# Kernel optimization log

Measured on AMD Instinct MI355X. Metric: run time of the kernel, lower is better.

The kernel has to match this reference:

```python
import jax, jax.numpy as jnp
import numpy as np

MARGIN = 0.2
EPS = 1e-12  # F.normalize eps


def _l2norm(x, axis):
    n = jnp.linalg.norm(x, axis=axis, keepdims=True)
    return x / jnp.maximum(n, EPS)


def setup_inputs() -> dict:
    key = jax.random.key(0)
    k1, k2, k3, k4 = jax.random.split(key, 4)
    B, L_im, L_s, D = 256, 37, 33, 1024
    im_set = jax.random.normal(k1, (B, L_im, D), dtype=jnp.float32)
    s_seq = jax.random.normal(k2, (B, L_s, D), dtype=jnp.float32)
    # realistic valid lengths (>= a few regions/words, <= max)
    im_len = jax.random.randint(k3, (B,), 10, L_im + 1, dtype=jnp.int32)
    s_len = jax.random.randint(k4, (B,), 8, L_s + 1, dtype=jnp.int32)
    return {"im_set": im_set, "s_seq": s_seq, "im_len": im_len, "s_len": s_len}


def _aggr_similarity(im_set, s_seq, im_len, s_len):
    # l2-normalize feature dim, then drop CLS region / special tokens
    im = _l2norm(im_set, axis=2)[:, 1:, :]          # [B, Li, D]
    s = _l2norm(s_seq, axis=2)[:, 1:-2, :]          # [B, Ls, D]
    im_l = im_len - 1
    s_l = s_len - 3
    Li, Ls = im.shape[1], s.shape[1]
    # cross-batch alignment scores: [B_im, B_s, Li, Ls]
    align = jnp.einsum('bid,cjd->bcij', im, s)
    im_invalid = jnp.arange(Li)[None, :] >= im_l[:, None]   # [B, Li]
    s_invalid = jnp.arange(Ls)[None, :] >= s_l[:, None]     # [B, Ls]
    mask = im_invalid[:, None, :, None] | s_invalid[None, :, None, :]
    align = jnp.where(mask, 0.0, align)
    # 'MrSw': max over image regions, sum over sentence words
    return align.max(axis=2).sum(axis=2)             # [B_im, B_s]


def _contrastive_loss(scores):
    B = scores.shape[0]
    diag = jnp.diagonal(scores)                      # [B]
    cost_s = jnp.maximum(MARGIN + scores - diag[:, None], 0.0)
    cost_im = jnp.maximum(MARGIN + scores - diag[None, :], 0.0)
    eye = jnp.eye(B, dtype=bool)
    cost_s = jnp.where(eye, 0.0, cost_s)
    cost_im = jnp.where(eye, 0.0, cost_im)
    # max_violation=True: hardest negatives
    return cost_s.max(axis=1).sum() + cost_im.max(axis=0).sum()


def reference(im_set, s_seq, im_len, s_len):
    scores = _aggr_similarity(im_set, s_seq, im_len, s_len)
    return _contrastive_loss(scores)
```

## Files before the change

### kernel.cpp

```cpp
#include <hip/hip_runtime.h>
#include <hip/hip_bf16.h>


typedef __attribute__((ext_vector_type(8))) short bf16x8;
typedef __attribute__((ext_vector_type(4))) float f32x4;

#define NB   256
#define DIM  1024
#define LI   36
#define LIP  36
#define LS   30
#define LSP  32

static __device__ inline ushort f2bf(float x) {
    union { __hip_bfloat16 h; ushort u; } cvt;
    cvt.h = __float2bfloat16(x);
    return cvt.u;
}

static __device__ __forceinline__ void gload_lds16(const void* g, void* l) {
    __builtin_amdgcn_global_load_lds(
        (const __attribute__((address_space(1))) void*)g,
        (__attribute__((address_space(3))) void*)l, 16, 0, 0);
}

__global__ __launch_bounds__(256) void normalize_pack(
    const float* __restrict__ im, const float* __restrict__ sq,
    short* __restrict__ imp, short* __restrict__ sp)
{
    const int gw   = (blockIdx.x * 256 + threadIdx.x) >> 6;
    const int lane = threadIdx.x & 63;
    const int NIM  = NB * LI;

    const float* src[2];
    short* dst[2];
    #pragma unroll
    for (int rr = 0; rr < 2; ++rr) {
        const int row = gw * 2 + rr;
        if (row < NIM) {
            int b = row / LI, i = row - b * LI;
            dst[rr] = imp + (size_t)row * DIM;
            src[rr] = im + ((size_t)b * 37 + i + 1) * DIM;
        } else {
            int g2 = row - NIM;
            int b = g2 >> 5, j = g2 & 31;
            dst[rr] = sp + (size_t)g2 * DIM;
            src[rr] = (j < LS) ? (sq + ((size_t)b * 33 + j + 1) * DIM)
                               : nullptr;
        }
    }

    float4 v[2][4];
    float ss[2] = {0.f, 0.f};
    #pragma unroll
    for (int rr = 0; rr < 2; ++rr) {
        if (src[rr]) {
            const float4* s4 = (const float4*)src[rr];
            #pragma unroll
            for (int t = 0; t < 4; ++t) {
                float4 x = s4[lane + 64 * t];
                v[rr][t] = x;
                ss[rr] += x.x * x.x + x.y * x.y + x.z * x.z + x.w * x.w;
            }
        }
    }
    #pragma unroll
    for (int o = 32; o >= 1; o >>= 1) {
        ss[0] += __shfl_xor(ss[0], o, 64);
        ss[1] += __shfl_xor(ss[1], o, 64);
    }
    #pragma unroll
    for (int rr = 0; rr < 2; ++rr) {
        if (src[rr]) {
            const float scale = 1.0f / fmaxf(sqrtf(ss[rr]), 1e-12f);
            ushort4* d4 = (ushort4*)dst[rr];
            #pragma unroll
            for (int t = 0; t < 4; ++t) {
                float4 x = v[rr][t];
                ushort4 o;
                o.x = f2bf(x.x * scale);
                o.y = f2bf(x.y * scale);
                o.z = f2bf(x.z * scale);
                o.w = f2bf(x.w * scale);
                d4[lane + 64 * t] = o;
            }
        } else {
            uint4 z = {0u, 0u, 0u, 0u};
            uint4* d4 = (uint4*)dst[rr];
            d4[lane] = z;
            d4[lane + 64] = z;
        }
    }
}

__global__ __launch_bounds__(256, 2) void gemm_scores(
    const short* __restrict__ imp, const short* __restrict__ sp,
    const int* __restrict__ im_len, const int* __restrict__ s_len,
    float* __restrict__ scores)
{
    __shared__ short As[144 * 64];
    __shared__ short Bs[256 * 64];

    const int tid  = threadIdx.x;
    const int wave = tid >> 6;
    const int lane = tid & 63;
    const int q    = lane >> 4;
    const int l15  = lane & 15;
    const int b0   = blockIdx.x * 4;
    const int c0   = blockIdx.y * 8;

    f32x4 acc[9][4];
    #pragma unroll
    for (int mt = 0; mt < 9; ++mt)
        #pragma unroll
        for (int t = 0; t < 4; ++t)
            acc[mt][t] = (f32x4){0.f, 0.f, 0.f, 0.f};

    const int srow   = lane >> 3;
    const int schunk = (lane & 7) ^ srow;
    const char* gA = (const char*)imp + (size_t)(b0 * LIP) * 2048
                     + srow * 2048 + schunk * 16;
    const char* gB = (const char*)sp + (size_t)(c0 * LSP) * 2048
                     + srow * 2048 + schunk * 16;

    const int cs0 = ((q)     ^ (l15 & 7)) * 16;
    const int cs1 = ((4 + q) ^ (l15 & 7)) * 16;

    const int wa4 = wave * 4;
    const int wb8 = wave * 8;

    for (int k0 = 0; k0 < DIM; k0 += 64) {
        const int kb = k0 * 2;
        #pragma unroll
        for (int it = 0; it < 4; ++it) {
            const int rb = wa4 + it;
            gload_lds16(gA + rb * (8 * 2048) + kb, (char*)As + rb * 1024);
        }
        if (wave < 2) {
            const int rb = 16 + wave;
            gload_lds16(gA + rb * (8 * 2048) + kb, (char*)As + rb * 1024);
        }
        #pragma unroll
        for (int it = 0; it < 8; ++it) {
            const int rb = wb8 + it;
            gload_lds16(gB + rb * (8 * 2048) + kb, (char*)Bs + rb * 1024);
        }
        __syncthreads();
        #pragma unroll
        for (int g = 0; g < 2; ++g) {
            const int cs = g ? cs1 : cs0;
            bf16x8 af[9], bfr[4];
            #pragma unroll
            for (int mt = 0; mt < 9; ++mt)
                af[mt] = *(const bf16x8*)((const char*)As + (mt * 16 + l15) * 128 + cs);
            #pragma unroll
            for (int t = 0; t < 4; ++t)
                bfr[t] = *(const bf16x8*)((const char*)Bs + ((wave * 4 + t) * 16 + l15) * 128 + cs);
            #pragma unroll
            for (int mt = 0; mt < 9; ++mt)
                #pragma unroll
                for (int t = 0; t < 4; ++t)
                    acc[mt][t] = __builtin_amdgcn_mfma_f32_16x16x32_bf16(
                        af[mt], bfr[t], acc[mt][t], 0, 0, 0);
        }
        __syncthreads();
    }

    int il[4];
    #pragma unroll
    for (int bb = 0; bb < 4; ++bb) il[bb] = im_len[b0 + bb] - 1;

    float sc[4][2] = {{0.f,0.f},{0.f,0.f},{0.f,0.f},{0.f,0.f}};
    #pragma unroll
    for (int t = 0; t < 4; ++t) {
        const int nt = wave * 4 + t;
        const int c  = c0 + (nt >> 1);
        const int sl = s_len[c] - 3;
        const int jj = (nt & 1) * 16 + l15;
        const bool jv = (jj < sl);

        float m[4] = {-3.4e38f, -3.4e38f, -3.4e38f, -3.4e38f};
        #pragma unroll
        for (int mt = 0; mt < 9; ++mt) {
            const int im_lo = (4 * mt) / 9;
            const int im_hi = (4 * mt + 3) / 9;
            const int thr   = 9 * im_hi - 4 * mt;
            #pragma unroll
            for (int r = 0; r < 4; ++r) {
                const float v = acc[mt][t][r];
                const int base = mt * 16 + q * 4 + r;
                if (im_lo == im_hi) {
                    const int i = base - 36 * im_lo;
                    if (i < il[im_lo]) m[im_lo] = fmaxf(m[im_lo], v);
                } else {
                    const bool hi = (q >= thr);
                    if (!hi) {
                        const int i = base - 36 * im_lo;
                        if (i < il[im_lo]) m[im_lo] = fmaxf(m[im_lo], v);
                    } else {
                        const int i = base - 36 * im_hi;
                        if (i < il[im_hi]) m[im_hi] = fmaxf(m[im_hi], v);
                    }
                }
            }
        }
        #pragma unroll
        for (int bb = 0; bb < 4; ++bb) {
            float mm = m[bb];
            mm = fmaxf(mm, __shfl_xor(mm, 16, 64));
            mm = fmaxf(mm, __shfl_xor(mm, 32, 64));
            if (il[bb] < LI) mm = fmaxf(mm, 0.f);
            float v = (q == 0 && jv) ? mm : 0.f;
            #pragma unroll
            for (int off = 32; off >= 1; off >>= 1) v += __shfl_xor(v, off, 64);
            sc[bb][t >> 1] += v;
        }
    }
    if (lane == 0) {
        #pragma unroll
        for (int bb = 0; bb < 4; ++bb)
            #pragma unroll
            for (int h = 0; h < 2; ++h)
                scores[(b0 + bb) * NB + c0 + wave * 2 + h] = sc[bb][h];
    }
}

__global__ __launch_bounds__(256) void loss_fused(
    const float* __restrict__ sc, float* __restrict__ out)
{
    const int wave = threadIdx.x >> 6, lane = threadIdx.x & 63;
    const int t = blockIdx.x * 4 + wave;
    const float dt = sc[t * (NB + 1)];
    float rowmax = 0.f, colmax = 0.f;
    #pragma unroll
    for (int p = 0; p < 4; ++p) {
        const int k = lane + 64 * p;
        const float r = sc[t * NB + k];
        const float c = sc[k * NB + t];
        if (k != t) {
            rowmax = fmaxf(rowmax, 0.2f + r - dt);
            colmax = fmaxf(colmax, 0.2f + c - dt);
        }
    }
    #pragma unroll
    for (int o = 32; o >= 1; o >>= 1) {
        rowmax = fmaxf(rowmax, __shfl_xor(rowmax, o, 64));
        colmax = fmaxf(colmax, __shfl_xor(colmax, o, 64));
    }
    __shared__ float red[4];
    if (lane == 0) red[wave] = fmaxf(rowmax, 0.f) + fmaxf(colmax, 0.f);
    __syncthreads();
    if (threadIdx.x == 0)
        atomicAdd(out, red[0] + red[1] + red[2] + red[3]);
}

extern "C" void kernel_launch(void* const* d_in, const int* in_sizes, int n_in,
                              void* d_out, int out_size, void* d_ws, size_t ws_size,
                              hipStream_t stream) {
    const float* im_set = (const float*)d_in[0];
    const float* s_seq  = (const float*)d_in[1];
    const int*   im_len = (const int*)d_in[2];
    const int*   s_len  = (const int*)d_in[3];
    float* out = (float*)d_out;

    char* ws = (char*)d_ws;
    const size_t imp_bytes = (size_t)NB * LIP * DIM * 2;
    const size_t sp_bytes  = (size_t)NB * LSP * DIM * 2;
    short* imp    = (short*)ws;
    short* sp     = (short*)(ws + imp_bytes);
    float* scores = (float*)(ws + imp_bytes + sp_bytes);

    normalize_pack<<<2176, 256, 0, stream>>>(im_set, s_seq, imp, sp);

    dim3 grid(NB / 4, NB / 8);
    gemm_scores<<<grid, 256, 0, stream>>>(imp, sp, im_len, s_len, scores);

    loss_fused<<<64, 256, 0, stream>>>(scores, out);
}
```

Before: 238.2 us.

## Double gemm block tile to 8 images x 8 sentences with 8 waves

```diff
diff --git a/kernel.cpp b/kernel.cpp
--- a/kernel.cpp
+++ b/kernel.cpp
@@ -93,12 +93,12 @@
     }
 }
 
-__global__ __launch_bounds__(256, 2) void gemm_scores(
+__global__ __launch_bounds__(512, 2) void gemm_scores(
     const short* __restrict__ imp, const short* __restrict__ sp,
     const int* __restrict__ im_len, const int* __restrict__ s_len,
     float* __restrict__ scores)
 {
-    __shared__ short As[144 * 64];
+    __shared__ short As[288 * 64];
     __shared__ short Bs[256 * 64];
 
     const int tid  = threadIdx.x;
@@ -106,7 +106,9 @@
     const int lane = tid & 63;
     const int q    = lane >> 4;
     const int l15  = lane & 15;
-    const int b0   = blockIdx.x * 4;
+    const int wm   = wave >> 2;
+    const int wn   = wave & 3;
+    const int b0   = blockIdx.x * 8;
     const int c0   = blockIdx.y * 8;
 
     f32x4 acc[9][4];
@@ -126,24 +128,19 @@
     const int cs0 = ((q)     ^ (l15 & 7)) * 16;
     const int cs1 = ((4 + q) ^ (l15 & 7)) * 16;
 
-    const int wa4 = wave * 4;
-    const int wb8 = wave * 8;
+    const int arow0 = wm * 144;
 
     for (int k0 = 0; k0 < DIM; k0 += 64) {
         const int kb = k0 * 2;
         #pragma unroll
-        for (int it = 0; it < 4; ++it) {
-            const int rb = wa4 + it;
-            gload_lds16(gA + rb * (8 * 2048) + kb, (char*)As + rb * 1024);
-        }
-        if (wave < 2) {
-            const int rb = 16 + wave;
-            gload_lds16(gA + rb * (8 * 2048) + kb, (char*)As + rb * 1024);
-        }
-        #pragma unroll
-        for (int it = 0; it < 8; ++it) {
-            const int rb = wb8 + it;
-            gload_lds16(gB + rb * (8 * 2048) + kb, (char*)Bs + rb * 1024);
+        for (int j = 0; j < 9; ++j) {
+            const int cid = wave + 8 * j;
+            if (cid < 36) {
+                gload_lds16(gA + cid * (8 * 2048) + kb, (char*)As + cid * 1024);
+            } else if (cid < 68) {
+                const int bc = cid - 36;
+                gload_lds16(gB + bc * (8 * 2048) + kb, (char*)Bs + bc * 1024);
+            }
         }
         __syncthreads();
         #pragma unroll
@@ -152,10 +149,10 @@
             bf16x8 af[9], bfr[4];
             #pragma unroll
             for (int mt = 0; mt < 9; ++mt)
-                af[mt] = *(const bf16x8*)((const char*)As + (mt * 16 + l15) * 128 + cs);
+                af[mt] = *(const bf16x8*)((const char*)As + (arow0 + mt * 16 + l15) * 128 + cs);
             #pragma unroll
             for (int t = 0; t < 4; ++t)
-                bfr[t] = *(const bf16x8*)((const char*)Bs + ((wave * 4 + t) * 16 + l15) * 128 + cs);
+                bfr[t] = *(const bf16x8*)((const char*)Bs + ((wn * 4 + t) * 16 + l15) * 128 + cs);
             #pragma unroll
             for (int mt = 0; mt < 9; ++mt)
                 #pragma unroll
@@ -166,17 +163,17 @@
         __syncthreads();
     }
 
+    const int b0w = b0 + wm * 4;
     int il[4];
     #pragma unroll
-    for (int bb = 0; bb < 4; ++bb) il[bb] = im_len[b0 + bb] - 1;
+    for (int bb = 0; bb < 4; ++bb) il[bb] = im_len[b0w + bb] - 1;
 
     float sc[4][2] = {{0.f,0.f},{0.f,0.f},{0.f,0.f},{0.f,0.f}};
     #pragma unroll
     for (int t = 0; t < 4; ++t) {
-        const int nt = wave * 4 + t;
-        const int c  = c0 + (nt >> 1);
+        const int c  = c0 + wn * 2 + (t >> 1);
         const int sl = s_len[c] - 3;
-        const int jj = (nt & 1) * 16 + l15;
+        const int jj = (t & 1) * 16 + l15;
         const bool jv = (jj < sl);
 
         float m[4] = {-3.4e38f, -3.4e38f, -3.4e38f, -3.4e38f};
@@ -221,7 +218,7 @@
         for (int bb = 0; bb < 4; ++bb)
             #pragma unroll
             for (int h = 0; h < 2; ++h)
-                scores[(b0 + bb) * NB + c0 + wave * 2 + h] = sc[bb][h];
+                scores[(b0w + bb) * NB + c0 + wn * 2 + h] = sc[bb][h];
     }
 }
 
@@ -272,8 +269,8 @@
 
     normalize_pack<<<2176, 256, 0, stream>>>(im_set, s_seq, imp, sp);
 
-    dim3 grid(NB / 4, NB / 8);
-    gemm_scores<<<grid, 256, 0, stream>>>(imp, sp, im_len, s_len, scores);
+    dim3 grid(NB / 8, NB / 8);
+    gemm_scores<<<grid, 512, 0, stream>>>(imp, sp, im_len, s_len, scores);
 
     loss_fused<<<64, 256, 0, stream>>>(scores, out);
 }
```

Measured after the change: 264.5 us. 1.11x slower.

## Double-buffer LDS K-slices so global loads overlap MFMA compute

Applied to the files above, without the earlier changes.

```diff
diff --git a/kernel.cpp b/kernel.cpp
--- a/kernel.cpp
+++ b/kernel.cpp
@@ -11,6 +11,9 @@
 #define LIP  36
 #define LS   30
 #define LSP  32
+#define ABYTES 9216
+#define BUFB   25600
+#define NSLICE 32
 
 static __device__ inline ushort f2bf(float x) {
     union { __hip_bfloat16 h; ushort u; } cvt;
@@ -98,8 +101,7 @@
     const int* __restrict__ im_len, const int* __restrict__ s_len,
     float* __restrict__ scores)
 {
-    __shared__ short As[144 * 64];
-    __shared__ short Bs[256 * 64];
+    __shared__ __align__(1024) char lds[2 * BUFB];
 
     const int tid  = threadIdx.x;
     const int wave = tid >> 6;
@@ -116,54 +118,63 @@
         for (int t = 0; t < 4; ++t)
             acc[mt][t] = (f32x4){0.f, 0.f, 0.f, 0.f};
 
-    const int srow   = lane >> 3;
-    const int schunk = (lane & 7) ^ srow;
-    const char* gA = (const char*)imp + (size_t)(b0 * LIP) * 2048
-                     + srow * 2048 + schunk * 16;
-    const char* gB = (const char*)sp + (size_t)(c0 * LSP) * 2048
-                     + srow * 2048 + schunk * 16;
-
-    const int cs0 = ((q)     ^ (l15 & 7)) * 16;
-    const int cs1 = ((4 + q) ^ (l15 & 7)) * 16;
-
-    const int wa4 = wave * 4;
-    const int wb8 = wave * 8;
-
-    for (int k0 = 0; k0 < DIM; k0 += 64) {
-        const int kb = k0 * 2;
-        #pragma unroll
-        for (int it = 0; it < 4; ++it) {
-            const int rb = wa4 + it;
-            gload_lds16(gA + rb * (8 * 2048) + kb, (char*)As + rb * 1024);
-        }
-        if (wave < 2) {
-            const int rb = 16 + wave;
-            gload_lds16(gA + rb * (8 * 2048) + kb, (char*)As + rb * 1024);
-        }
-        #pragma unroll
-        for (int it = 0; it < 8; ++it) {
-            const int rb = wb8 + it;
-            gload_lds16(gB + rb * (8 * 2048) + kb, (char*)Bs + rb * 1024);
-        }
+    const int i8 = lane >> 3;
+    const int ph = lane & 7;
+    const int sl = ph ^ i8;
+    const int off_lane = (2 * i8 + (sl >> 2)) * 2048 + (sl & 3) * 16;
+
+    const char* baseA = (const char*)imp + (size_t)(b0 * LIP) * 2048;
+    const char* baseB = (const char*)sp  + (size_t)(c0 * LSP) * 2048;
+
+    const char* g7[7];
+    int l7[7];
+    #pragma unroll
+    for (int j = 0; j < 7; ++j) {
+        const int cid = wave + 4 * j;
+        if (cid < 9) {
+            g7[j] = baseA + cid * (16 * 2048) + off_lane;
+            l7[j] = cid * 1024;
+        } else {
+            const int bc = (cid < 25 ? cid : 9) - 9;
+            g7[j] = baseB + bc * (16 * 2048) + off_lane;
+            l7[j] = ABYTES + bc * 1024;
+        }
+    }
+    const int nst = (wave == 0) ? 7 : 6;
+
+    const int cs2 = (((l15 & 1) * 4 + q) ^ ((l15 >> 1) & 7)) * 16;
+    const int lhalf = l15 >> 1;
+
+    auto compute = [&](const char* buf) {
+        bf16x8 af[9], bfr[4];
+        #pragma unroll
+        for (int mt = 0; mt < 9; ++mt)
+            af[mt] = *(const bf16x8*)(buf + (8 * mt + lhalf) * 128 + cs2);
+        #pragma unroll
+        for (int t = 0; t < 4; ++t)
+            bfr[t] = *(const bf16x8*)(buf + ABYTES + (8 * (wave * 4 + t) + lhalf) * 128 + cs2);
+        #pragma unroll
+        for (int mt = 0; mt < 9; ++mt)
+            #pragma unroll
+            for (int t = 0; t < 4; ++t)
+                acc[mt][t] = __builtin_amdgcn_mfma_f32_16x16x32_bf16(
+                    af[mt], bfr[t], acc[mt][t], 0, 0, 0);
+    };
+
+    for (int j = 0; j < nst; ++j) gload_lds16(g7[j], lds + l7[j]);
+    __syncthreads();
+
+    int cur = 0;
+    #pragma unroll 1
+    for (int kk = 0; kk < NSLICE; ++kk) {
+        if (kk < NSLICE - 1) {
+            const int nb = cur ^ 1;
+            for (int j = 0; j < nst; ++j)
+                gload_lds16(g7[j] + (kk + 1) * 64, lds + nb * BUFB + l7[j]);
+        }
+        compute(lds + cur * BUFB);
         __syncthreads();
-        #pragma unroll
-        for (int g = 0; g < 2; ++g) {
-            const int cs = g ? cs1 : cs0;
-            bf16x8 af[9], bfr[4];
-            #pragma unroll
-            for (int mt = 0; mt < 9; ++mt)
-                af[mt] = *(const bf16x8*)((const char*)As + (mt * 16 + l15) * 128 + cs);
-            #pragma unroll
-            for (int t = 0; t < 4; ++t)
-                bfr[t] = *(const bf16x8*)((const char*)Bs + ((wave * 4 + t) * 16 + l15) * 128 + cs);
-            #pragma unroll
-            for (int mt = 0; mt < 9; ++mt)
-                #pragma unroll
-                for (int t = 0; t < 4; ++t)
-                    acc[mt][t] = __builtin_amdgcn_mfma_f32_16x16x32_bf16(
-                        af[mt], bfr[t], acc[mt][t], 0, 0, 0);
-        }
-        __syncthreads();
+        cur ^= 1;
     }
 
     int il[4];
@@ -175,9 +186,9 @@
     for (int t = 0; t < 4; ++t) {
         const int nt = wave * 4 + t;
         const int c  = c0 + (nt >> 1);
-        const int sl = s_len[c] - 3;
+        const int sl2 = s_len[c] - 3;
         const int jj = (nt & 1) * 16 + l15;
-        const bool jv = (jj < sl);
+        const bool jv = (jj < sl2);
 
         float m[4] = {-3.4e38f, -3.4e38f, -3.4e38f, -3.4e38f};
         #pragma unroll
```

New measurement: 309.2 us. 29.8% more time.
